# Performance work log

Hardware: AMD Instinct MI355X
Metric: run time of the kernel (lower is better)

## Reference

```python
import jax, jax.numpy as jnp
import numpy as np

D = 1024
H = 16
HD = D // H
C = 50000


def setup_inputs() -> dict:
    key = jax.random.key(0)
    ks = jax.random.split(key, 16)
    s = 0.02
    return {
        "nodes": jax.random.normal(ks[0], (C, D), dtype=jnp.float32),
        "z_prev": jax.random.normal(ks[1], (D,), dtype=jnp.float32),
        "Wq": jax.random.normal(ks[2], (D, D), dtype=jnp.float32) * s,
        "bq": jnp.zeros((D,), dtype=jnp.float32),
        "Wk": jax.random.normal(ks[3], (D, D), dtype=jnp.float32) * s,
        "bk": jnp.zeros((D,), dtype=jnp.float32),
        "Wv": jax.random.normal(ks[4], (D, D), dtype=jnp.float32) * s,
        "bv": jnp.zeros((D,), dtype=jnp.float32),
        "W1": jax.random.normal(ks[5], (2 * D, D), dtype=jnp.float32) * s,
        "b1": jnp.zeros((D,), dtype=jnp.float32),
        "W2": jax.random.normal(ks[6], (D, D), dtype=jnp.float32) * s,
        "b2": jnp.zeros((D,), dtype=jnp.float32),
        "scale": jnp.ones((D,), dtype=jnp.float32),
    }


def _rmsnorm(x, scale, eps=1e-6):
    # matches torch: scale * x * rsqrt(mean(x^2) + eps)
    ms = jnp.mean(jnp.square(x), axis=-1, keepdims=True)
    return scale * x * jax.lax.rsqrt(ms + eps)


def reference(nodes, z_prev, Wq, bq, Wk, bk, Wv, bv, W1, b1, W2, b2, scale):
    # projections (weights stored [in, out])
    Q = (z_prev @ Wq + bq).reshape(H, HD)          # [H, hd]
    K = (nodes @ Wk + bk).reshape(C, H, HD)        # [C, H, hd]
    V = (nodes @ Wv + bv).reshape(C, H, HD)        # [C, H, hd]
    # single-query multi-head attention over C nodes
    scores = jnp.einsum("hd,chd->hc", Q, K) / np.sqrt(HD).astype(np.float32)
    weights = jax.nn.softmax(scores, axis=-1)      # [H, C]
    pooled = jnp.einsum("hc,chd->hd", weights, V).reshape(D)
    # concat -> MLP (GELU exact, matching torch nn.GELU default) -> RMSNorm
    z = jnp.concatenate([pooled, z_prev], axis=-1)  # [2D]
    h = jax.nn.gelu(z @ W1 + b1, approximate=False)
    z_out = _rmsnorm(h @ W2 + b2, scale)
    return z_out
```

## Files before the change

kernel.cpp:

```cpp
#include <hip/hip_runtime.h>
#include <hip/hip_bf16.h>
#include <math.h>

#define C_N 50000

typedef float f32x16 __attribute__((ext_vector_type(16)));
typedef float f32x4v __attribute__((ext_vector_type(4)));
typedef short bf16x8 __attribute__((ext_vector_type(8)));
typedef unsigned short u16x4 __attribute__((ext_vector_type(4)));
#define VZERO16 {0.f,0.f,0.f,0.f,0.f,0.f,0.f,0.f,0.f,0.f,0.f,0.f,0.f,0.f,0.f,0.f}

#define OQ     0
#define OZ     1024
#define OH1P   3072
#define OY     5120
#define OSUMB  6144
#define OQKB   14336
#define OPP2   22528
#define OPP    284672

__device__ __forceinline__ int brev4(int l){
  return ((l&1)<<3)|((l&2)<<1)|((l&4)>>1)|((l&8)>>3);
}

__device__ __forceinline__ float bf2f(unsigned short u){
  unsigned int x = ((unsigned int)u)<<16;
  return __builtin_bit_cast(float, x);
}

__device__ __forceinline__ float vred16(f32x16 v, int lane){
  float send, got;
#define RS(A,B,M) \
  send = (lane&M)? v[A] : v[B]; \
  got  = __shfl_xor(send, M);   \
  v[A] = ((lane&M)? v[B] : v[A]) + got;
  RS(0,8,1) RS(1,9,1) RS(2,10,1) RS(3,11,1)
  RS(4,12,1) RS(5,13,1) RS(6,14,1) RS(7,15,1)
  RS(0,4,2) RS(1,5,2) RS(2,6,2) RS(3,7,2)
  RS(0,2,4) RS(1,3,4)
  RS(0,1,8)
#undef RS
  float t = v[0];
  t += __shfl_xor(t,16);
  t += __shfl_xor(t,32);
  return t;
}

template<int IN, int NT>
__device__ __forceinline__ float mv_dot(const float* __restrict__ W,
    const float* __restrict__ x, int tid, int jblk){
  __shared__ float xs[IN];
  __shared__ float red[NT/16][17];
  for (int k=tid;k<IN;k+=NT) xs[k]=x[k];
  __syncthreads();
  int jq = tid&15, iq = tid>>4;
  int j = jblk*16 + jq;
  float acc = 0.f;
#pragma unroll 8
  for (int i=iq;i<IN;i+=NT/16)
    acc = fmaf(xs[i], W[(size_t)i*1024 + j], acc);
  red[iq][jq] = acc;
  __syncthreads();
  float s = 0.f;
  if (tid < 16){
#pragma unroll
    for (int ii=0;ii<NT/16;ii++) s += red[ii][tid];
  }
  return s;
}

__global__ __launch_bounds__(1024) void hm_mvQ(const float* __restrict__ W,
    const float* __restrict__ x, const float* __restrict__ bq,
    float* __restrict__ Q, float* __restrict__ z){
  float s = mv_dot<1024,1024>(W, x, threadIdx.x, blockIdx.x);
  int tid = threadIdx.x;
  int j0 = blockIdx.x*16;
  if (tid < 16){
    Q[j0+tid] = s + bq[j0+tid];
    z[1024 + j0 + tid] = x[j0 + tid];
  }
}

__global__ __launch_bounds__(256) void hm_qk2(const float* __restrict__ Wk,
    const float* __restrict__ Q, unsigned short* __restrict__ qkb){
  __shared__ float qlds[1024];
  int tid = threadIdx.x;
  for (int k=tid;k<1024;k+=256) qlds[k]=Q[k];
  __syncthreads();
  int w = tid>>6, l = tid&63;
  int i = blockIdx.x*4 + w;
  const float* wr = Wk + (size_t)i*1024 + l;
  f32x16 acc = VZERO16;
#define QKS(k) acc[k] = wr[k*64] * qlds[k*64 + l];
  QKS(0) QKS(1) QKS(2) QKS(3) QKS(4) QKS(5) QKS(6) QKS(7)
  QKS(8) QKS(9) QKS(10) QKS(11) QKS(12) QKS(13) QKS(14) QKS(15)
#undef QKS
  float t = vred16(acc, l);
  if (l < 16){
    int h = brev4(l);
    int kc = i>>5, rg = (i>>3)&3, jj = i&7;
    __hip_bfloat16 b = __float2bfloat16(t);
    qkb[(kc*64 + rg*16 + h)*8 + jj] = *(unsigned short*)&b;
  }
}

#define LD2(AP,KC,FA,FB) \
  FA = *(const float4*)((AP)+(KC)*32); \
  FB = *(const float4*)((AP)+(KC)*32+4);
#define CVT8(FA,FB,AV) { \
  __hip_bfloat16 c0=__float2bfloat16(FA.x),c1=__float2bfloat16(FA.y); \
  __hip_bfloat16 c2=__float2bfloat16(FA.z),c3=__float2bfloat16(FA.w); \
  __hip_bfloat16 c4=__float2bfloat16(FB.x),c5=__float2bfloat16(FB.y); \
  __hip_bfloat16 c6=__float2bfloat16(FB.z),c7=__float2bfloat16(FB.w); \
  AV[0]=*(short*)&c0; AV[1]=*(short*)&c1; AV[2]=*(short*)&c2; AV[3]=*(short*)&c3; \
  AV[4]=*(short*)&c4; AV[5]=*(short*)&c5; AV[6]=*(short*)&c6; AV[7]=*(short*)&c7; }

__global__ __launch_bounds__(256,2) void hm_fused(const float* __restrict__ nodes,
    const unsigned short* __restrict__ qkb, unsigned short* __restrict__ parts,
    float* __restrict__ sumpb){
  extern __shared__ float tile[];
  __shared__ float part[4][16][17];
  __shared__ float eb[16][16];
  const int tid = threadIdx.x, w = tid>>6, l = tid&63;
  const int rowA = l&15, kgrp = l>>4;
  const int r_ = tid>>4, h_ = tid&15;

  bf16x8 bq0,bq1,bq2,bq3,bq4,bq5,bq6,bq7;
  {
    const bf16x8* qb = (const bf16x8*)qkb;
    const int o = w*8*64 + l;
    bq0=qb[o]; bq1=qb[o+64]; bq2=qb[o+128]; bq3=qb[o+192];
    bq4=qb[o+256]; bq5=qb[o+320]; bq6=qb[o+384]; bq7=qb[o+448];
  }
  f32x16 a0 = VZERO16, a1 = VZERO16, a2 = VZERO16, a3 = VZERO16;
  float ssum = 0.f;
  const int stride = gridDim.x;

  int cb = blockIdx.x;
  float4 p0a,p0b,p1a,p1b,p2a,p2b,p3a,p3b,p4a,p4b,p5a,p5b,p6a,p6b,p7a,p7b;
  {
    const float* ap = nodes + ((size_t)(cb*16 + rowA))*1024 + w*256 + kgrp*8;
    LD2(ap,0,p0a,p0b) LD2(ap,1,p1a,p1b) LD2(ap,2,p2a,p2b) LD2(ap,3,p3a,p3b)
    LD2(ap,4,p4a,p4b) LD2(ap,5,p5a,p5b) LD2(ap,6,p6a,p6b) LD2(ap,7,p7a,p7b)
  }
  float* tw = tile + rowA*1028 + w*256 + kgrp*8;

  for (; cb < 3125; cb += stride){
    *(float4*)(tw+0*32) = p0a; *(float4*)(tw+0*32+4) = p0b;
    *(float4*)(tw+1*32) = p1a; *(float4*)(tw+1*32+4) = p1b;
    *(float4*)(tw+2*32) = p2a; *(float4*)(tw+2*32+4) = p2b;
    *(float4*)(tw+3*32) = p3a; *(float4*)(tw+3*32+4) = p3b;
    *(float4*)(tw+4*32) = p4a; *(float4*)(tw+4*32+4) = p4b;
    *(float4*)(tw+5*32) = p5a; *(float4*)(tw+5*32+4) = p5b;
    *(float4*)(tw+6*32) = p6a; *(float4*)(tw+6*32+4) = p6b;
    *(float4*)(tw+7*32) = p7a; *(float4*)(tw+7*32+4) = p7b;
    bf16x8 av0,av1,av2,av3,av4,av5,av6,av7;
    CVT8(p0a,p0b,av0) CVT8(p1a,p1b,av1) CVT8(p2a,p2b,av2) CVT8(p3a,p3b,av3)
    CVT8(p4a,p4b,av4) CVT8(p5a,p5b,av5) CVT8(p6a,p6b,av6) CVT8(p7a,p7b,av7)
    f32x4v D0 = {0.f,0.f,0.f,0.f};
    f32x4v D1 = {0.f,0.f,0.f,0.f};
    D0 = __builtin_amdgcn_mfma_f32_16x16x32_bf16(av0, bq0, D0, 0,0,0);
    D1 = __builtin_amdgcn_mfma_f32_16x16x32_bf16(av1, bq1, D1, 0,0,0);
    D0 = __builtin_amdgcn_mfma_f32_16x16x32_bf16(av2, bq2, D0, 0,0,0);
    D1 = __builtin_amdgcn_mfma_f32_16x16x32_bf16(av3, bq3, D1, 0,0,0);
    D0 = __builtin_amdgcn_mfma_f32_16x16x32_bf16(av4, bq4, D0, 0,0,0);
    D1 = __builtin_amdgcn_mfma_f32_16x16x32_bf16(av5, bq5, D1, 0,0,0);
    D0 = __builtin_amdgcn_mfma_f32_16x16x32_bf16(av6, bq6, D0, 0,0,0);
    D1 = __builtin_amdgcn_mfma_f32_16x16x32_bf16(av7, bq7, D1, 0,0,0);
    {
      int cbn = cb + stride; if (cbn >= 3125) cbn = cb;
      const float* apn = nodes + ((size_t)(cbn*16 + rowA))*1024 + w*256 + kgrp*8;
      LD2(apn,0,p0a,p0b) LD2(apn,1,p1a,p1b) LD2(apn,2,p2a,p2b) LD2(apn,3,p3a,p3b)
      LD2(apn,4,p4a,p4b) LD2(apn,5,p5a,p5b) LD2(apn,6,p6a,p6b) LD2(apn,7,p7a,p7b)
    }
#pragma unroll
    for (int i=0;i<4;i++) part[w][kgrp*4+i][rowA] = D0[i] + D1[i];
    __syncthreads();
    {
      float s = part[0][r_][h_]+part[1][r_][h_]+part[2][r_][h_]+part[3][r_][h_];
      eb[r_][h_] = __expf(s * 0.125f);
    }
    __syncthreads();
    if (tid < 16){
#pragma unroll
      for (int rr=0;rr<16;rr++) ssum += eb[rr][tid];
    }
    const float* tr = tile + w*256 + l*4;
#pragma unroll 4
    for (int r=0;r<16;r++){
      float4 nv = *(const float4*)(tr + r*1028);
      f32x16 u = *(const f32x16*)&eb[r][0];
      a0 += u*nv.x; a1 += u*nv.y; a2 += u*nv.z; a3 += u*nv.w;
    }
  }
  unsigned short* p = parts + (size_t)blockIdx.x*16384 + w*256 + l*4;
#pragma unroll
  for (int h=0;h<16;h++){
    __hip_bfloat16 b0=__float2bfloat16(a0[h]), b1=__float2bfloat16(a1[h]);
    __hip_bfloat16 b2=__float2bfloat16(a2[h]), b3=__float2bfloat16(a3[h]);
    u16x4 o;
    o[0]=*(unsigned short*)&b0; o[1]=*(unsigned short*)&b1;
    o[2]=*(unsigned short*)&b2; o[3]=*(unsigned short*)&b3;
    *(u16x4*)(p + h*1024) = o;
  }
  if (tid < 16) sumpb[blockIdx.x*16 + tid] = ssum;
}

__global__ __launch_bounds__(256) void hm_predA(const unsigned short* __restrict__ parts,
    unsigned short* __restrict__ pp2, int nb){
  int j4 = blockIdx.x*256 + threadIdx.x;
  int b0 = blockIdx.y*16;
  int b1 = b0+16 < nb ? b0+16 : nb;
  float s0=0.f, s1=0.f, s2=0.f, s3=0.f;
  for (int b=b0;b<b1;b++){
    u16x4 v = *(const u16x4*)&parts[(size_t)b*16384 + j4*4];
    s0 += bf2f(v[0]); s1 += bf2f(v[1]); s2 += bf2f(v[2]); s3 += bf2f(v[3]);
  }
  __hip_bfloat16 r0=__float2bfloat16(s0), r1=__float2bfloat16(s1);
  __hip_bfloat16 r2=__float2bfloat16(s2), r3=__float2bfloat16(s3);
  u16x4 o;
  o[0]=*(unsigned short*)&r0; o[1]=*(unsigned short*)&r1;
  o[2]=*(unsigned short*)&r2; o[3]=*(unsigned short*)&r3;
  *(u16x4*)&pp2[(size_t)blockIdx.y*16384 + j4*4] = o;
}

__global__ __launch_bounds__(1024) void hm_mvV(const float* __restrict__ W,
    const unsigned short* __restrict__ pp2, const float* __restrict__ sumpb,
    const float* __restrict__ bv, float* __restrict__ z, int ny, int nb){
  __shared__ float xs[1024];
  __shared__ float red[64][17];
  __shared__ float ssl[16];
  const int tid = threadIdx.x;
  const int hh = blockIdx.x>>2;
  float sacc = 0.f;
  for (int b=tid; b<nb; b+=1024) sacc += sumpb[b*16 + hh];
#pragma unroll
  for (int m=1;m<64;m<<=1) sacc += __shfl_xor(sacc, m);
  if ((tid&63)==0) ssl[tid>>6] = sacc;
  {
    int k = tid;
    float s = 0.f;
    for (int y=0;y<ny;y++) s += bf2f(pp2[(size_t)y*16384 + hh*1024 + k]);
    xs[k] = s;
  }
  __syncthreads();
  int jq = tid&15, iq = tid>>4;
  int j = blockIdx.x*16 + jq;
  float acc = 0.f;
#pragma unroll 8
  for (int i=iq;i<1024;i+=64)
    acc = fmaf(xs[i], W[(size_t)i*1024 + j], acc);
  red[iq][jq] = acc;
  __syncthreads();
  if (tid < 16){
    float s = 0.f;
#pragma unroll
    for (int ii=0;ii<64;ii++) s += red[ii][tid];
    float S = 0.f;
#pragma unroll
    for (int q=0;q<16;q++) S += ssl[q];
    int jo = blockIdx.x*16 + tid;
    z[jo] = s / S + bv[jo];
  }
}

__global__ __launch_bounds__(1024) void hm_mvW1(const float* __restrict__ W,
    const float* __restrict__ z, float* __restrict__ h1part){
  __shared__ float xs[1024];
  __shared__ float red[64][17];
  const int tid = threadIdx.x;
  const int iseg = blockIdx.y;
  xs[tid] = z[iseg*1024 + tid];
  __syncthreads();
  int jq = tid&15, iq = tid>>4;
  int j = blockIdx.x*16 + jq;
  const float* Wp = W + (size_t)(iseg*1024)*1024;
  float acc = 0.f;
#pragma unroll
  for (int k=0;k<16;k++){
    int i = iq + 64*k;
    acc = fmaf(xs[i], Wp[(size_t)i*1024 + j], acc);
  }
  red[iq][jq] = acc;
  __syncthreads();
  if (tid < 16){
    float s = 0.f;
#pragma unroll
    for (int ii=0;ii<64;ii++) s += red[ii][tid];
    h1part[iseg*1024 + blockIdx.x*16 + tid] = s;
  }
}

__global__ __launch_bounds__(1024) void hm_mvW2(const float* __restrict__ W,
    const float* __restrict__ h1part, const float* __restrict__ b1,
    const float* __restrict__ b2, float* __restrict__ y){
  __shared__ float xs[1024];
  __shared__ float red[64][17];
  const int tid = threadIdx.x;
  {
    float s = b1[tid] + h1part[tid] + h1part[1024 + tid];
    xs[tid] = 0.5f * s * (1.0f + erff(s * 0.70710678118654752f));
  }
  __syncthreads();
  int jq = tid&15, iq = tid>>4;
  int j = blockIdx.x*16 + jq;
  float acc = 0.f;
#pragma unroll
  for (int k=0;k<16;k++){
    int i = iq + 64*k;
    acc = fmaf(xs[i], W[(size_t)i*1024 + j], acc);
  }
  red[iq][jq] = acc;
  __syncthreads();
  if (tid < 16){
    float s = 0.f;
#pragma unroll
    for (int ii=0;ii<64;ii++) s += red[ii][tid];
    int jo = blockIdx.x*16 + tid;
    y[jo] = s + b2[jo];
  }
}

__global__ __launch_bounds__(256) void hm_rms(const float* __restrict__ y,
    const float* __restrict__ scale, float* __restrict__ out){
  __shared__ float red[4];
  __shared__ float msv;
  int tid = threadIdx.x;
  float local = 0.f;
  for (int j=tid;j<1024;j+=256){ float t = y[j]; local = fmaf(t,t,local); }
#pragma unroll
  for (int m=1;m<64;m<<=1) local += __shfl_xor(local, m);
  if ((tid&63)==0) red[tid>>6] = local;
  __syncthreads();
  if (tid==0){
    float s = red[0]+red[1]+red[2]+red[3];
    msv = rsqrtf(s*(1.0f/1024.0f) + 1e-6f);
  }
  __syncthreads();
  float r = msv;
  for (int j=tid;j<1024;j+=256) out[j] = scale[j]*y[j]*r;
}

extern "C" void kernel_launch(void* const* d_in, const int* in_sizes, int n_in,
                              void* d_out, int out_size, void* d_ws, size_t ws_size,
                              hipStream_t stream){
  const float* nodes  = (const float*)d_in[0];
  const float* z_prev = (const float*)d_in[1];
  const float* Wq = (const float*)d_in[2];
  const float* bq = (const float*)d_in[3];
  const float* Wk = (const float*)d_in[4];
  const float* Wv = (const float*)d_in[6];
  const float* bv = (const float*)d_in[7];
  const float* W1 = (const float*)d_in[8];
  const float* b1 = (const float*)d_in[9];
  const float* W2 = (const float*)d_in[10];
  const float* b2 = (const float*)d_in[11];
  const float* scale = (const float*)d_in[12];
  float* ws  = (float*)d_ws;
  float* out = (float*)d_out;

  float* Qv     = ws + OQ;
  float* z      = ws + OZ;
  float* h1part = ws + OH1P;
  float* ybuf   = ws + OY;
  float* sumb   = ws + OSUMB;
  unsigned short* qkb = (unsigned short*)(ws + OQKB);
  unsigned short* pp2 = (unsigned short*)(ws + OPP2);
  unsigned short* pp  = (unsigned short*)(ws + OPP);

  size_t need0 = (size_t)OPP*4;
  int nbp = 1;
  if (ws_size > need0 + 32768) nbp = (int)((ws_size - need0)/32768);
  if (nbp > 512) nbp = 512;
  if (nbp < 1) nbp = 1;
  int ny = (nbp + 15)/16;

  const size_t tile_bytes = 16*1028*sizeof(float);

  hm_mvQ   <<<64,  1024, 0, stream>>>(Wq, z_prev, bq, Qv, z);
  hm_qk2   <<<256, 256, 0, stream>>>(Wk, Qv, qkb);
  hm_fused <<<nbp, 256, tile_bytes, stream>>>(nodes, qkb, pp, sumb);
  hm_predA <<<dim3(16,ny), 256, 0, stream>>>(pp, pp2, nbp);
  hm_mvV   <<<64,  1024, 0, stream>>>(Wv, pp2, sumb, bv, z, ny, nbp);
  hm_mvW1  <<<dim3(64,2), 1024, 0, stream>>>(W1, z, h1part);
  hm_mvW2  <<<64,  1024, 0, stream>>>(W2, h1part, b1, b2, ybuf);
  hm_rms   <<<1,   256, 0, stream>>>(ybuf, scale, out);
}
```

Measured before the change: 87.49 us.

## Split matvec kernels along the input dimension for more blocks and fold reductions downstream

Splits the Q, V and W2 matrix-vector kernels along the input dimension into more, smaller blocks (256 blocks of 256 threads, or 128 blocks) that write partial sums. The partial sums, biases and normalisation are then summed in the consuming kernel (qk2, mvW1, rms). The softmax denominator reduction moves into predA. The aim is better occupancy and memory-level parallelism on the bandwidth-bound weight reads, and removing the serial tail loops of the 1024-thread single-pass kernels. The cost is extra partial-sum traffic and redundant summation in the consumers.

New measurement: 92.27 us. +5.5%, slower.

```diff
diff --git a/kernel.cpp b/kernel.cpp
--- a/kernel.cpp
+++ b/kernel.cpp
@@ -10,14 +10,15 @@
 typedef unsigned short u16x4 __attribute__((ext_vector_type(4)));
 #define VZERO16 {0.f,0.f,0.f,0.f,0.f,0.f,0.f,0.f,0.f,0.f,0.f,0.f,0.f,0.f,0.f,0.f}
 
-#define OQ     0
-#define OZ     1024
-#define OH1P   3072
-#define OY     5120
-#define OSUMB  6144
-#define OQKB   14336
-#define OPP2   22528
-#define OPP    284672
+#define OQP    0
+#define OZP    4096
+#define OH1P   8192
+#define OY2P   10240
+#define OSS    12288
+#define OSUMB  12304
+#define OQKB   20496
+#define OPP2   28688
+#define OPP    290832
 
 __device__ __forceinline__ int brev4(int l){
   return ((l&1)<<3)|((l&2)<<1)|((l&4)>>1)|((l&8)>>3);
@@ -46,46 +47,38 @@
   return t;
 }
 
-template<int IN, int NT>
-__device__ __forceinline__ float mv_dot(const float* __restrict__ W,
-    const float* __restrict__ x, int tid, int jblk){
-  __shared__ float xs[IN];
-  __shared__ float red[NT/16][17];
-  for (int k=tid;k<IN;k+=NT) xs[k]=x[k];
+__global__ __launch_bounds__(256) void hm_mvQp(const float* __restrict__ W,
+    const float* __restrict__ x, float* __restrict__ qp){
+  __shared__ float xs[256];
+  __shared__ float red[16][17];
+  const int tid = threadIdx.x, jblk = blockIdx.x, iseg = blockIdx.y;
+  xs[tid] = x[iseg*256 + tid];
   __syncthreads();
   int jq = tid&15, iq = tid>>4;
-  int j = jblk*16 + jq;
+  const float* Wp = W + (size_t)(iseg*256)*1024 + jblk*16 + jq;
   float acc = 0.f;
-#pragma unroll 8
-  for (int i=iq;i<IN;i+=NT/16)
-    acc = fmaf(xs[i], W[(size_t)i*1024 + j], acc);
+#pragma unroll
+  for (int k=0;k<16;k++){
+    int i = iq + 16*k;
+    acc = fmaf(xs[i], Wp[(size_t)i*1024], acc);
+  }
   red[iq][jq] = acc;
   __syncthreads();
-  float s = 0.f;
   if (tid < 16){
-#pragma unroll
-    for (int ii=0;ii<NT/16;ii++) s += red[ii][tid];
-  }
-  return s;
-}
-
-__global__ __launch_bounds__(1024) void hm_mvQ(const float* __restrict__ W,
-    const float* __restrict__ x, const float* __restrict__ bq,
-    float* __restrict__ Q, float* __restrict__ z){
-  float s = mv_dot<1024,1024>(W, x, threadIdx.x, blockIdx.x);
-  int tid = threadIdx.x;
-  int j0 = blockIdx.x*16;
-  if (tid < 16){
-    Q[j0+tid] = s + bq[j0+tid];
-    z[1024 + j0 + tid] = x[j0 + tid];
+    float s = 0.f;
+#pragma unroll
+    for (int ii=0;ii<16;ii++) s += red[ii][tid];
+    qp[iseg*1024 + jblk*16 + tid] = s;
   }
 }
 
 __global__ __launch_bounds__(256) void hm_qk2(const float* __restrict__ Wk,
-    const float* __restrict__ Q, unsigned short* __restrict__ qkb){
+    const float* __restrict__ qp, const float* __restrict__ bq,
+    unsigned short* __restrict__ qkb){
   __shared__ float qlds[1024];
   int tid = threadIdx.x;
-  for (int k=tid;k<1024;k+=256) qlds[k]=Q[k];
+  for (int k=tid;k<1024;k+=256)
+    qlds[k] = bq[k] + qp[k] + qp[1024+k] + qp[2048+k] + qp[3072+k];
   __syncthreads();
   int w = tid>>6, l = tid&63;
   int i = blockIdx.x*4 + w;
@@ -207,7 +200,9 @@
 }
 
 __global__ __launch_bounds__(256) void hm_predA(const unsigned short* __restrict__ parts,
-    unsigned short* __restrict__ pp2, int nb){
+    unsigned short* __restrict__ pp2, const float* __restrict__ sumpb,
+    float* __restrict__ S, int nb){
+  __shared__ float red[16][17];
   int j4 = blockIdx.x*256 + threadIdx.x;
   int b0 = blockIdx.y*16;
   int b1 = b0+16 < nb ? b0+16 : nb;
@@ -222,64 +217,73 @@
   o[0]=*(unsigned short*)&r0; o[1]=*(unsigned short*)&r1;
   o[2]=*(unsigned short*)&r2; o[3]=*(unsigned short*)&r3;
   *(u16x4*)&pp2[(size_t)blockIdx.y*16384 + j4*4] = o;
-}
-
-__global__ __launch_bounds__(1024) void hm_mvV(const float* __restrict__ W,
-    const unsigned short* __restrict__ pp2, const float* __restrict__ sumpb,
-    const float* __restrict__ bv, float* __restrict__ z, int ny, int nb){
+  if (blockIdx.x == 0 && blockIdx.y == 0){
+    int tid = threadIdx.x, h = tid&15, g = tid>>4;
+    float sp = 0.f;
+    for (int b=g; b<nb; b+=16) sp += sumpb[b*16 + h];
+    red[g][h] = sp;
+    __syncthreads();
+    if (tid < 16){
+      float sv = 0.f;
+#pragma unroll
+      for (int gg=0; gg<16; gg++) sv += red[gg][tid];
+      S[tid] = sv;
+    }
+  }
+}
+
+__global__ __launch_bounds__(256) void hm_mvVp(const float* __restrict__ W,
+    const unsigned short* __restrict__ pp2, float* __restrict__ zpart, int ny){
+  __shared__ float xs[256];
+  __shared__ float red[16][17];
+  const int tid = threadIdx.x, jblk = blockIdx.x, iseg = blockIdx.y;
+  const int hh = jblk>>2;
+  {
+    float s = 0.f;
+    int base = hh*1024 + iseg*256 + tid;
+    for (int y=0;y<ny;y++) s += bf2f(pp2[(size_t)y*16384 + base]);
+    xs[tid] = s;
+  }
+  __syncthreads();
+  int jq = tid&15, iq = tid>>4;
+  const float* Wp = W + (size_t)(iseg*256)*1024 + jblk*16 + jq;
+  float acc = 0.f;
+#pragma unroll
+  for (int k=0;k<16;k++){
+    int i = iq + 16*k;
+    acc = fmaf(xs[i], Wp[(size_t)i*1024], acc);
+  }
+  red[iq][jq] = acc;
+  __syncthreads();
+  if (tid < 16){
+    float s = 0.f;
+#pragma unroll
+    for (int ii=0;ii<16;ii++) s += red[ii][tid];
+    zpart[iseg*1024 + jblk*16 + tid] = s;
+  }
+}
+
+__global__ __launch_bounds__(1024) void hm_mvW1(const float* __restrict__ W,
+    const float* __restrict__ zpart, const float* __restrict__ S,
+    const float* __restrict__ bv, const float* __restrict__ z_prev,
+    float* __restrict__ h1part){
   __shared__ float xs[1024];
   __shared__ float red[64][17];
-  __shared__ float ssl[16];
-  const int tid = threadIdx.x;
-  const int hh = blockIdx.x>>2;
-  float sacc = 0.f;
-  for (int b=tid; b<nb; b+=1024) sacc += sumpb[b*16 + hh];
-#pragma unroll
-  for (int m=1;m<64;m<<=1) sacc += __shfl_xor(sacc, m);
-  if ((tid&63)==0) ssl[tid>>6] = sacc;
-  {
-    int k = tid;
-    float s = 0.f;
-    for (int y=0;y<ny;y++) s += bf2f(pp2[(size_t)y*16384 + hh*1024 + k]);
-    xs[k] = s;
+  const int tid = threadIdx.x, jblk = blockIdx.x, iseg = blockIdx.y;
+  if (iseg == 0){
+    float s = zpart[tid]+zpart[1024+tid]+zpart[2048+tid]+zpart[3072+tid];
+    xs[tid] = s / S[tid>>6] + bv[tid];
+  } else {
+    xs[tid] = z_prev[tid];
   }
   __syncthreads();
   int jq = tid&15, iq = tid>>4;
-  int j = blockIdx.x*16 + jq;
-  float acc = 0.f;
-#pragma unroll 8
-  for (int i=iq;i<1024;i+=64)
-    acc = fmaf(xs[i], W[(size_t)i*1024 + j], acc);
-  red[iq][jq] = acc;
-  __syncthreads();
-  if (tid < 16){
-    float s = 0.f;
-#pragma unroll
-    for (int ii=0;ii<64;ii++) s += red[ii][tid];
-    float S = 0.f;
-#pragma unroll
-    for (int q=0;q<16;q++) S += ssl[q];
-    int jo = blockIdx.x*16 + tid;
-    z[jo] = s / S + bv[jo];
-  }
-}
-
-__global__ __launch_bounds__(1024) void hm_mvW1(const float* __restrict__ W,
-    const float* __restrict__ z, float* __restrict__ h1part){
-  __shared__ float xs[1024];
-  __shared__ float red[64][17];
-  const int tid = threadIdx.x;
-  const int iseg = blockIdx.y;
-  xs[tid] = z[iseg*1024 + tid];
-  __syncthreads();
-  int jq = tid&15, iq = tid>>4;
-  int j = blockIdx.x*16 + jq;
-  const float* Wp = W + (size_t)(iseg*1024)*1024;
+  const float* Wp = W + (size_t)(iseg*1024)*1024 + jblk*16 + jq;
   float acc = 0.f;
 #pragma unroll
   for (int k=0;k<16;k++){
     int i = iq + 64*k;
-    acc = fmaf(xs[i], Wp[(size_t)i*1024 + j], acc);
+    acc = fmaf(xs[i], Wp[(size_t)i*1024], acc);
   }
   red[iq][jq] = acc;
   __syncthreads();
@@ -287,28 +291,29 @@
     float s = 0.f;
 #pragma unroll
     for (int ii=0;ii<64;ii++) s += red[ii][tid];
-    h1part[iseg*1024 + blockIdx.x*16 + tid] = s;
+    h1part[iseg*1024 + jblk*16 + tid] = s;
   }
 }
 
 __global__ __launch_bounds__(1024) void hm_mvW2(const float* __restrict__ W,
     const float* __restrict__ h1part, const float* __restrict__ b1,
-    const float* __restrict__ b2, float* __restrict__ y){
-  __shared__ float xs[1024];
+    float* __restrict__ y2part){
+  __shared__ float xs[512];
   __shared__ float red[64][17];
-  const int tid = threadIdx.x;
-  {
-    float s = b1[tid] + h1part[tid] + h1part[1024 + tid];
+  const int tid = threadIdx.x, jblk = blockIdx.x, iseg = blockIdx.y;
+  if (tid < 512){
+    int ii = iseg*512 + tid;
+    float s = b1[ii] + h1part[ii] + h1part[1024 + ii];
     xs[tid] = 0.5f * s * (1.0f + erff(s * 0.70710678118654752f));
   }
   __syncthreads();
   int jq = tid&15, iq = tid>>4;
-  int j = blockIdx.x*16 + jq;
+  const float* Wp = W + (size_t)(iseg*512)*1024 + jblk*16 + jq;
   float acc = 0.f;
 #pragma unroll
-  for (int k=0;k<16;k++){
+  for (int k=0;k<8;k++){
     int i = iq + 64*k;
-    acc = fmaf(xs[i], W[(size_t)i*1024 + j], acc);
+    acc = fmaf(xs[i], Wp[(size_t)i*1024], acc);
   }
   red[iq][jq] = acc;
   __syncthreads();
@@ -316,29 +321,32 @@
     float s = 0.f;
 #pragma unroll
     for (int ii=0;ii<64;ii++) s += red[ii][tid];
-    int jo = blockIdx.x*16 + tid;
-    y[jo] = s + b2[jo];
-  }
-}
-
-__global__ __launch_bounds__(256) void hm_rms(const float* __restrict__ y,
-    const float* __restrict__ scale, float* __restrict__ out){
-  __shared__ float red[4];
+    y2part[iseg*1024 + jblk*16 + tid] = s;
+  }
+}
+
+__global__ __launch_bounds__(1024) void hm_rms(const float* __restrict__ y2part,
+    const float* __restrict__ b2, const float* __restrict__ scale,
+    float* __restrict__ out){
+  __shared__ float yb[1024];
+  __shared__ float rr[16];
   __shared__ float msv;
   int tid = threadIdx.x;
-  float local = 0.f;
-  for (int j=tid;j<1024;j+=256){ float t = y[j]; local = fmaf(t,t,local); }
-#pragma unroll
-  for (int m=1;m<64;m<<=1) local += __shfl_xor(local, m);
-  if ((tid&63)==0) red[tid>>6] = local;
+  float y = b2[tid] + y2part[tid] + y2part[1024 + tid];
+  yb[tid] = y;
+  float loc = y*y;
+#pragma unroll
+  for (int m=1;m<64;m<<=1) loc += __shfl_xor(loc, m);
+  if ((tid&63)==0) rr[tid>>6] = loc;
   __syncthreads();
   if (tid==0){
-    float s = red[0]+red[1]+red[2]+red[3];
+    float s = 0.f;
+#pragma unroll
+    for (int q=0;q<16;q++) s += rr[q];
     msv = rsqrtf(s*(1.0f/1024.0f) + 1e-6f);
   }
   __syncthreads();
-  float r = msv;
-  for (int j=tid;j<1024;j+=256) out[j] = scale[j]*y[j]*r;
+  out[tid] = scale[tid]*yb[tid]*msv;
 }
 
 extern "C" void kernel_launch(void* const* d_in, const int* in_sizes, int n_in,
@@ -359,10 +367,11 @@
   float* ws  = (float*)d_ws;
   float* out = (float*)d_out;
 
-  float* Qv     = ws + OQ;
-  float* z      = ws + OZ;
+  float* qp     = ws + OQP;
+  float* zpart  = ws + OZP;
   float* h1part = ws + OH1P;
-  float* ybuf   = ws + OY;
+  float* y2part = ws + OY2P;
+  float* Sv     = ws + OSS;
   float* sumb   = ws + OSUMB;
   unsigned short* qkb = (unsigned short*)(ws + OQKB);
   unsigned short* pp2 = (unsigned short*)(ws + OPP2);
@@ -377,12 +386,12 @@
 
   const size_t tile_bytes = 16*1028*sizeof(float);
 
-  hm_mvQ   <<<64,  1024, 0, stream>>>(Wq, z_prev, bq, Qv, z);
-  hm_qk2   <<<256, 256, 0, stream>>>(Wk, Qv, qkb);
+  hm_mvQp  <<<dim3(64,4), 256, 0, stream>>>(Wq, z_prev, qp);
+  hm_qk2   <<<256, 256, 0, stream>>>(Wk, qp, bq, qkb);
   hm_fused <<<nbp, 256, tile_bytes, stream>>>(nodes, qkb, pp, sumb);
-  hm_predA <<<dim3(16,ny), 256, 0, stream>>>(pp, pp2, nbp);
-  hm_mvV   <<<64,  1024, 0, stream>>>(Wv, pp2, sumb, bv, z, ny, nbp);
-  hm_mvW1  <<<dim3(64,2), 1024, 0, stream>>>(W1, z, h1part);
-  hm_mvW2  <<<64,  1024, 0, stream>>>(W2, h1part, b1, b2, ybuf);
-  hm_rms   <<<1,   256, 0, stream>>>(ybuf, scale, out);
-}
+  hm_predA <<<dim3(16,ny), 256, 0, stream>>>(pp, pp2, sumb, Sv, nbp);
+  hm_mvVp  <<<dim3(64,4), 256, 0, stream>>>(Wv, pp2, zpart, ny);
+  hm_mvW1  <<<dim3(64,2), 1024, 0, stream>>>(W1, zpart, Sv, bv, z_prev, h1part);
+  hm_mvW2  <<<dim3(64,2), 1024, 0, stream>>>(W2, h1part, b1, y2part);
+  hm_rms   <<<1, 1024, 0, stream>>>(y2part, b2, scale, out);
+}
```

## Fuse cross-block partial reduction into attention kernel via global atomic barrier

Applied to the files above, without the earlier changes.

Removes the separate hm_predA reduction kernel. After writing its bf16 partials, each hm_fused block joins a grid-wide barrier built on an atomic counter, then helps reduce all partials into a float Pu buffer that hm_mvV reads directly. This saves one kernel launch and the intermediate bf16 pp2 round trip, and mvV no longer loops over ny. The barrier only works if all nbp blocks (up to 512, two per CU) are resident at once, and the spinning adds tail latency.

Result: slower. 221.6 us (+153.2%).

```diff
diff --git a/kernel.cpp b/kernel.cpp
--- a/kernel.cpp
+++ b/kernel.cpp
@@ -14,10 +14,11 @@
 #define OZ     1024
 #define OH1P   3072
 #define OY     5120
-#define OSUMB  6144
-#define OQKB   14336
-#define OPP2   22528
-#define OPP    284672
+#define OCTR   6144
+#define OSUMB  6160
+#define OQKB   14352
+#define OPU    22544
+#define OPP    38928
 
 __device__ __forceinline__ int brev4(int l){
   return ((l&1)<<3)|((l&2)<<1)|((l&4)>>1)|((l&8)>>3);
@@ -71,7 +72,8 @@
 
 __global__ __launch_bounds__(1024) void hm_mvQ(const float* __restrict__ W,
     const float* __restrict__ x, const float* __restrict__ bq,
-    float* __restrict__ Q, float* __restrict__ z){
+    float* __restrict__ Q, float* __restrict__ z, int* __restrict__ ctr){
+  if (blockIdx.x==0 && threadIdx.x==0) *ctr = 0;
   float s = mv_dot<1024,1024>(W, x, threadIdx.x, blockIdx.x);
   int tid = threadIdx.x;
   int j0 = blockIdx.x*16;
@@ -117,10 +119,11 @@
 
 __global__ __launch_bounds__(256,2) void hm_fused(const float* __restrict__ nodes,
     const unsigned short* __restrict__ qkb, unsigned short* __restrict__ parts,
-    float* __restrict__ sumpb){
+    float* __restrict__ sumpb, float* __restrict__ Pu, int* __restrict__ ctr){
   extern __shared__ float tile[];
   __shared__ float part[4][16][17];
   __shared__ float eb[16][16];
+  __shared__ float rsum[8][32];
   const int tid = threadIdx.x, w = tid>>6, l = tid&63;
   const int rowA = l&15, kgrp = l>>4;
   const int r_ = tid>>4, h_ = tid&15;
@@ -204,29 +207,37 @@
     *(u16x4*)(p + h*1024) = o;
   }
   if (tid < 16) sumpb[blockIdx.x*16 + tid] = ssum;
-}
-
-__global__ __launch_bounds__(256) void hm_predA(const unsigned short* __restrict__ parts,
-    unsigned short* __restrict__ pp2, int nb){
-  int j4 = blockIdx.x*256 + threadIdx.x;
-  int b0 = blockIdx.y*16;
-  int b1 = b0+16 < nb ? b0+16 : nb;
-  float s0=0.f, s1=0.f, s2=0.f, s3=0.f;
-  for (int b=b0;b<b1;b++){
-    u16x4 v = *(const u16x4*)&parts[(size_t)b*16384 + j4*4];
-    s0 += bf2f(v[0]); s1 += bf2f(v[1]); s2 += bf2f(v[2]); s3 += bf2f(v[3]);
-  }
-  __hip_bfloat16 r0=__float2bfloat16(s0), r1=__float2bfloat16(s1);
-  __hip_bfloat16 r2=__float2bfloat16(s2), r3=__float2bfloat16(s3);
-  u16x4 o;
-  o[0]=*(unsigned short*)&r0; o[1]=*(unsigned short*)&r1;
-  o[2]=*(unsigned short*)&r2; o[3]=*(unsigned short*)&r3;
-  *(u16x4*)&pp2[(size_t)blockIdx.y*16384 + j4*4] = o;
+  __threadfence();
+  __syncthreads();
+  if (tid == 0){
+    atomicAdd(ctr, 1);
+    while (__hip_atomic_load(ctr, __ATOMIC_ACQUIRE, __HIP_MEMORY_SCOPE_AGENT)
+           < (int)gridDim.x)
+      __builtin_amdgcn_s_sleep(2);
+  }
+  __syncthreads();
+  __threadfence();
+  const int nb = gridDim.x;
+  for (int j0 = blockIdx.x*32; j0 < 16384; j0 += nb*32){
+    int jj = tid&31, bgrp = tid>>5;
+    float s = 0.f;
+    for (int b=bgrp; b<nb; b+=8)
+      s += bf2f(parts[(size_t)b*16384 + j0 + jj]);
+    rsum[bgrp][jj] = s;
+    __syncthreads();
+    if (tid < 32){
+      float t = 0.f;
+#pragma unroll
+      for (int g=0; g<8; g++) t += rsum[g][tid];
+      Pu[j0 + tid] = t;
+    }
+    __syncthreads();
+  }
 }
 
 __global__ __launch_bounds__(1024) void hm_mvV(const float* __restrict__ W,
-    const unsigned short* __restrict__ pp2, const float* __restrict__ sumpb,
-    const float* __restrict__ bv, float* __restrict__ z, int ny, int nb){
+    const float* __restrict__ Pu, const float* __restrict__ sumpb,
+    const float* __restrict__ bv, float* __restrict__ z, int nb){
   __shared__ float xs[1024];
   __shared__ float red[64][17];
   __shared__ float ssl[16];
@@ -237,12 +248,7 @@
 #pragma unroll
   for (int m=1;m<64;m<<=1) sacc += __shfl_xor(sacc, m);
   if ((tid&63)==0) ssl[tid>>6] = sacc;
-  {
-    int k = tid;
-    float s = 0.f;
-    for (int y=0;y<ny;y++) s += bf2f(pp2[(size_t)y*16384 + hh*1024 + k]);
-    xs[k] = s;
-  }
+  xs[tid] = Pu[hh*1024 + tid];
   __syncthreads();
   int jq = tid&15, iq = tid>>4;
   int j = blockIdx.x*16 + jq;
@@ -363,9 +369,10 @@
   float* z      = ws + OZ;
   float* h1part = ws + OH1P;
   float* ybuf   = ws + OY;
+  int*   ctr    = (int*)(ws + OCTR);
   float* sumb   = ws + OSUMB;
   unsigned short* qkb = (unsigned short*)(ws + OQKB);
-  unsigned short* pp2 = (unsigned short*)(ws + OPP2);
+  float* Pu     = ws + OPU;
   unsigned short* pp  = (unsigned short*)(ws + OPP);
 
   size_t need0 = (size_t)OPP*4;
@@ -373,15 +380,13 @@
   if (ws_size > need0 + 32768) nbp = (int)((ws_size - need0)/32768);
   if (nbp > 512) nbp = 512;
   if (nbp < 1) nbp = 1;
-  int ny = (nbp + 15)/16;
 
   const size_t tile_bytes = 16*1028*sizeof(float);
 
-  hm_mvQ   <<<64,  1024, 0, stream>>>(Wq, z_prev, bq, Qv, z);
+  hm_mvQ   <<<64,  1024, 0, stream>>>(Wq, z_prev, bq, Qv, z, ctr);
   hm_qk2   <<<256, 256, 0, stream>>>(Wk, Qv, qkb);
-  hm_fused <<<nbp, 256, tile_bytes, stream>>>(nodes, qkb, pp, sumb);
-  hm_predA <<<dim3(16,ny), 256, 0, stream>>>(pp, pp2, nbp);
-  hm_mvV   <<<64,  1024, 0, stream>>>(Wv, pp2, sumb, bv, z, ny, nbp);
+  hm_fused <<<nbp, 256, tile_bytes, stream>>>(nodes, qkb, pp, sumb, Pu, ctr);
+  hm_mvV   <<<64,  1024, 0, stream>>>(Wv, Pu, sumb, bv, z, nbp);
   hm_mvW1  <<<dim3(64,2), 1024, 0, stream>>>(W1, z, h1part);
   hm_mvW2  <<<64,  1024, 0, stream>>>(W2, h1part, b1, b2, ybuf);
   hm_rms   <<<1,   256, 0, stream>>>(ybuf, scale, out);
```

## Fuse V-projection, MLP and RMSNorm tail into one kernel with grid barriers

Applied to the files above, without the earlier changes.

Replaces four tail launches (mvV, mvW1, mvW2, rms) with a single 64-block kernel that uses atomic-counter grid barriers between the stages. W1 now handles all 2048 inputs in each block and applies GELU inline, so the partial-sum buffer is gone. Counters are reset in hm_mvQ. The aim is to remove launch gaps on small matrix-vector stages. It relies on all 64 blocks being co-resident and adds spin-wait cost; the W1 stage also has half as many blocks streaming weights as before.

Result: slower. 180.4 us (+106.2%).

```diff
diff --git a/kernel.cpp b/kernel.cpp
--- a/kernel.cpp
+++ b/kernel.cpp
@@ -11,13 +11,14 @@
 #define VZERO16 {0.f,0.f,0.f,0.f,0.f,0.f,0.f,0.f,0.f,0.f,0.f,0.f,0.f,0.f,0.f,0.f}
 
 #define OQ     0
-#define OZ     1024
-#define OH1P   3072
-#define OY     5120
-#define OSUMB  6144
-#define OQKB   14336
-#define OPP2   22528
-#define OPP    284672
+#define OZB    1024
+#define OH1    2048
+#define OYB    3072
+#define OCTR   4096
+#define OSUMB  4112
+#define OQKB   12304
+#define OPP2   20496
+#define OPP    282640
 
 __device__ __forceinline__ int brev4(int l){
   return ((l&1)<<3)|((l&2)<<1)|((l&4)>>1)|((l&8)>>3);
@@ -46,6 +47,18 @@
   return t;
 }
 
+__device__ __forceinline__ void gbar(int* c, int n){
+  __syncthreads();
+  __threadfence();
+  if (threadIdx.x == 0){
+    atomicAdd(c, 1);
+    while (__hip_atomic_load(c, __ATOMIC_RELAXED, __HIP_MEMORY_SCOPE_AGENT) < n)
+      __builtin_amdgcn_s_sleep(1);
+  }
+  __syncthreads();
+  __threadfence();
+}
+
 template<int IN, int NT>
 __device__ __forceinline__ float mv_dot(const float* __restrict__ W,
     const float* __restrict__ x, int tid, int jblk){
@@ -71,14 +84,12 @@
 
 __global__ __launch_bounds__(1024) void hm_mvQ(const float* __restrict__ W,
     const float* __restrict__ x, const float* __restrict__ bq,
-    float* __restrict__ Q, float* __restrict__ z){
+    float* __restrict__ Q, int* __restrict__ ctr){
+  if (blockIdx.x==0 && threadIdx.x<3) ctr[threadIdx.x] = 0;
   float s = mv_dot<1024,1024>(W, x, threadIdx.x, blockIdx.x);
   int tid = threadIdx.x;
   int j0 = blockIdx.x*16;
-  if (tid < 16){
-    Q[j0+tid] = s + bq[j0+tid];
-    z[1024 + j0 + tid] = x[j0 + tid];
-  }
+  if (tid < 16) Q[j0+tid] = s + bq[j0+tid];
 }
 
 __global__ __launch_bounds__(256) void hm_qk2(const float* __restrict__ Wk,
@@ -224,121 +235,107 @@
   *(u16x4*)&pp2[(size_t)blockIdx.y*16384 + j4*4] = o;
 }
 
-__global__ __launch_bounds__(1024) void hm_mvV(const float* __restrict__ W,
+__global__ __launch_bounds__(1024) void hm_tail(const float* __restrict__ Wv,
     const unsigned short* __restrict__ pp2, const float* __restrict__ sumpb,
-    const float* __restrict__ bv, float* __restrict__ z, int ny, int nb){
-  __shared__ float xs[1024];
+    const float* __restrict__ bv, const float* __restrict__ z_prev,
+    const float* __restrict__ W1, const float* __restrict__ b1,
+    const float* __restrict__ W2, const float* __restrict__ b2,
+    const float* __restrict__ scale, float* __restrict__ zbuf,
+    float* __restrict__ h1buf, float* __restrict__ ybuf,
+    float* __restrict__ out, int ny, int nb, int* __restrict__ ctr){
+  __shared__ float xs[2048];
   __shared__ float red[64][17];
   __shared__ float ssl[16];
-  const int tid = threadIdx.x;
-  const int hh = blockIdx.x>>2;
-  float sacc = 0.f;
-  for (int b=tid; b<nb; b+=1024) sacc += sumpb[b*16 + hh];
-#pragma unroll
-  for (int m=1;m<64;m<<=1) sacc += __shfl_xor(sacc, m);
-  if ((tid&63)==0) ssl[tid>>6] = sacc;
-  {
-    int k = tid;
+  __shared__ float rr[16];
+  __shared__ float msv;
+  const int tid = threadIdx.x, bid = blockIdx.x;
+  const int jq = tid&15, iq = tid>>4;
+  const int j = bid*16 + jq;
+
+  {
+    const int hh = bid>>2;
+    float sacc = 0.f;
+    for (int b=tid; b<nb; b+=1024) sacc += sumpb[b*16 + hh];
+#pragma unroll
+    for (int m=1;m<64;m<<=1) sacc += __shfl_xor(sacc, m);
+    if ((tid&63)==0) ssl[tid>>6] = sacc;
     float s = 0.f;
-    for (int y=0;y<ny;y++) s += bf2f(pp2[(size_t)y*16384 + hh*1024 + k]);
-    xs[k] = s;
-  }
-  __syncthreads();
-  int jq = tid&15, iq = tid>>4;
-  int j = blockIdx.x*16 + jq;
-  float acc = 0.f;
+    for (int y=0;y<ny;y++) s += bf2f(pp2[(size_t)y*16384 + hh*1024 + tid]);
+    xs[tid] = s;
+    __syncthreads();
+    float acc = 0.f;
 #pragma unroll 8
-  for (int i=iq;i<1024;i+=64)
-    acc = fmaf(xs[i], W[(size_t)i*1024 + j], acc);
-  red[iq][jq] = acc;
-  __syncthreads();
-  if (tid < 16){
-    float s = 0.f;
-#pragma unroll
-    for (int ii=0;ii<64;ii++) s += red[ii][tid];
-    float S = 0.f;
-#pragma unroll
-    for (int q=0;q<16;q++) S += ssl[q];
-    int jo = blockIdx.x*16 + tid;
-    z[jo] = s / S + bv[jo];
-  }
-}
-
-__global__ __launch_bounds__(1024) void hm_mvW1(const float* __restrict__ W,
-    const float* __restrict__ z, float* __restrict__ h1part){
-  __shared__ float xs[1024];
-  __shared__ float red[64][17];
-  const int tid = threadIdx.x;
-  const int iseg = blockIdx.y;
-  xs[tid] = z[iseg*1024 + tid];
-  __syncthreads();
-  int jq = tid&15, iq = tid>>4;
-  int j = blockIdx.x*16 + jq;
-  const float* Wp = W + (size_t)(iseg*1024)*1024;
-  float acc = 0.f;
-#pragma unroll
-  for (int k=0;k<16;k++){
-    int i = iq + 64*k;
-    acc = fmaf(xs[i], Wp[(size_t)i*1024 + j], acc);
-  }
-  red[iq][jq] = acc;
-  __syncthreads();
-  if (tid < 16){
-    float s = 0.f;
-#pragma unroll
-    for (int ii=0;ii<64;ii++) s += red[ii][tid];
-    h1part[iseg*1024 + blockIdx.x*16 + tid] = s;
-  }
-}
-
-__global__ __launch_bounds__(1024) void hm_mvW2(const float* __restrict__ W,
-    const float* __restrict__ h1part, const float* __restrict__ b1,
-    const float* __restrict__ b2, float* __restrict__ y){
-  __shared__ float xs[1024];
-  __shared__ float red[64][17];
-  const int tid = threadIdx.x;
-  {
-    float s = b1[tid] + h1part[tid] + h1part[1024 + tid];
-    xs[tid] = 0.5f * s * (1.0f + erff(s * 0.70710678118654752f));
-  }
-  __syncthreads();
-  int jq = tid&15, iq = tid>>4;
-  int j = blockIdx.x*16 + jq;
-  float acc = 0.f;
-#pragma unroll
-  for (int k=0;k<16;k++){
-    int i = iq + 64*k;
-    acc = fmaf(xs[i], W[(size_t)i*1024 + j], acc);
-  }
-  red[iq][jq] = acc;
-  __syncthreads();
-  if (tid < 16){
-    float s = 0.f;
-#pragma unroll
-    for (int ii=0;ii<64;ii++) s += red[ii][tid];
-    int jo = blockIdx.x*16 + tid;
-    y[jo] = s + b2[jo];
-  }
-}
-
-__global__ __launch_bounds__(256) void hm_rms(const float* __restrict__ y,
-    const float* __restrict__ scale, float* __restrict__ out){
-  __shared__ float red[4];
-  __shared__ float msv;
-  int tid = threadIdx.x;
-  float local = 0.f;
-  for (int j=tid;j<1024;j+=256){ float t = y[j]; local = fmaf(t,t,local); }
-#pragma unroll
-  for (int m=1;m<64;m<<=1) local += __shfl_xor(local, m);
-  if ((tid&63)==0) red[tid>>6] = local;
-  __syncthreads();
-  if (tid==0){
-    float s = red[0]+red[1]+red[2]+red[3];
-    msv = rsqrtf(s*(1.0f/1024.0f) + 1e-6f);
-  }
-  __syncthreads();
-  float r = msv;
-  for (int j=tid;j<1024;j+=256) out[j] = scale[j]*y[j]*r;
+    for (int i=iq;i<1024;i+=64)
+      acc = fmaf(xs[i], Wv[(size_t)i*1024 + j], acc);
+    red[iq][jq] = acc;
+    __syncthreads();
+    if (tid < 16){
+      float s2 = 0.f;
+#pragma unroll
+      for (int ii=0;ii<64;ii++) s2 += red[ii][tid];
+      float S = 0.f;
+#pragma unroll
+      for (int q=0;q<16;q++) S += ssl[q];
+      int jo = bid*16 + tid;
+      zbuf[jo] = s2 / S + bv[jo];
+    }
+  }
+  gbar(ctr+0, gridDim.x);
+  {
+    xs[tid] = zbuf[tid];
+    xs[1024 + tid] = z_prev[tid];
+    __syncthreads();
+    float acc = 0.f;
+#pragma unroll 8
+    for (int i=iq;i<2048;i+=64)
+      acc = fmaf(xs[i], W1[(size_t)i*1024 + j], acc);
+    red[iq][jq] = acc;
+    __syncthreads();
+    if (tid < 16){
+      float s = 0.f;
+#pragma unroll
+      for (int ii=0;ii<64;ii++) s += red[ii][tid];
+      int jo = bid*16 + tid;
+      s += b1[jo];
+      h1buf[jo] = 0.5f * s * (1.0f + erff(s * 0.70710678118654752f));
+    }
+  }
+  gbar(ctr+1, gridDim.x);
+  {
+    __syncthreads();
+    xs[tid] = h1buf[tid];
+    __syncthreads();
+    float acc = 0.f;
+#pragma unroll 8
+    for (int i=iq;i<1024;i+=64)
+      acc = fmaf(xs[i], W2[(size_t)i*1024 + j], acc);
+    red[iq][jq] = acc;
+    __syncthreads();
+    if (tid < 16){
+      float s = 0.f;
+#pragma unroll
+      for (int ii=0;ii<64;ii++) s += red[ii][tid];
+      int jo = bid*16 + tid;
+      ybuf[jo] = s + b2[jo];
+    }
+  }
+  gbar(ctr+2, gridDim.x);
+  if (bid == 0){
+    float y = ybuf[tid];
+    float loc = y*y;
+#pragma unroll
+    for (int m=1;m<64;m<<=1) loc += __shfl_xor(loc, m);
+    if ((tid&63)==0) rr[tid>>6] = loc;
+    __syncthreads();
+    if (tid==0){
+      float s = 0.f;
+#pragma unroll
+      for (int q=0;q<16;q++) s += rr[q];
+      msv = rsqrtf(s*(1.0f/1024.0f) + 1e-6f);
+    }
+    __syncthreads();
+    out[tid] = scale[tid]*y*msv;
+  }
 }
 
 extern "C" void kernel_launch(void* const* d_in, const int* in_sizes, int n_in,
@@ -360,9 +357,10 @@
   float* out = (float*)d_out;
 
   float* Qv     = ws + OQ;
-  float* z      = ws + OZ;
-  float* h1part = ws + OH1P;
-  float* ybuf   = ws + OY;
+  float* zbuf   = ws + OZB;
+  float* h1buf  = ws + OH1;
+  float* ybuf   = ws + OYB;
+  int*   ctr    = (int*)(ws + OCTR);
   float* sumb   = ws + OSUMB;
   unsigned short* qkb = (unsigned short*)(ws + OQKB);
   unsigned short* pp2 = (unsigned short*)(ws + OPP2);
@@ -377,12 +375,11 @@
 
   const size_t tile_bytes = 16*1028*sizeof(float);
 
-  hm_mvQ   <<<64,  1024, 0, stream>>>(Wq, z_prev, bq, Qv, z);
+  hm_mvQ   <<<64,  1024, 0, stream>>>(Wq, z_prev, bq, Qv, ctr);
   hm_qk2   <<<256, 256, 0, stream>>>(Wk, Qv, qkb);
   hm_fused <<<nbp, 256, tile_bytes, stream>>>(nodes, qkb, pp, sumb);
   hm_predA <<<dim3(16,ny), 256, 0, stream>>>(pp, pp2, nbp);
-  hm_mvV   <<<64,  1024, 0, stream>>>(Wv, pp2, sumb, bv, z, ny, nbp);
-  hm_mvW1  <<<dim3(64,2), 1024, 0, stream>>>(W1, z, h1part);
-  hm_mvW2  <<<64,  1024, 0, stream>>>(W2, h1part, b1, b2, ybuf);
-  hm_rms   <<<1,   256, 0, stream>>>(ybuf, scale, out);
-}
+  hm_tail  <<<64,  1024, 0, stream>>>(Wv, pp2, sumb, bv, z_prev,
+                                      W1, b1, W2, b2, scale,
+                                      zbuf, h1buf, ybuf, out, ny, nbp, ctr);
+}
```
